# Optimization experiments

Measured on AMD Instinct MI355X. Metric: run time of the kernel, lower is better.

## Reference

```python
import jax, jax.numpy as jnp
from jax import lax
import numpy as np

B, N, C = 8, 16384, 128
NPOINT, NSAMPLE = 1024, 64
RADIUS = 0.3
MLP = [C + 3, 64, 64, 128]  # use_xyz adds 3 input channels


def furthest_point_sample(xyz, npoint):
    """xyz: (B, N, 3) -> inds: (B, npoint) int32, iterative FPS starting at index 0."""
    b, n, _ = xyz.shape
    init_idx = jnp.zeros((b,), jnp.int32)
    mind0 = jnp.full((b, n), 1e10, xyz.dtype)

    def step(carry, _):
        mind, last = carry
        p = jnp.take_along_axis(xyz, last[:, None, None], axis=1)  # (B,1,3)
        d = jnp.sum((xyz - p) ** 2, axis=-1)                       # (B,N)
        mind = jnp.minimum(mind, d)
        nxt = jnp.argmax(mind, axis=-1).astype(jnp.int32)
        return (mind, nxt), nxt

    (_, _), rest = lax.scan(step, (mind0, init_idx), None, length=npoint - 1)
    return jnp.concatenate([init_idx[None], rest], axis=0).T  # (B, npoint)


def ball_query(xyz, new_xyz, radius, nsample):
    """Return (B, npoint, nsample) indices: first nsample points within radius of
    each center; slots past the found count are filled with the first in-ball index
    (matches CUDA ball_query semantics)."""
    n = xyz.shape[1]
    d2 = jnp.sum((new_xyz[:, :, None, :] - xyz[:, None, :, :]) ** 2, axis=-1)  # (B,npoint,N)
    mask = d2 < radius * radius
    score = jnp.where(mask, -jnp.arange(n, dtype=jnp.int32), jnp.int32(-n))
    top, _ = lax.top_k(score, nsample)            # largest scores = smallest valid indices
    idx = -top
    valid = top > -n
    return jnp.where(valid, idx, idx[..., :1])    # pad with first in-ball index


def gather_points(x, idx):
    """x: (B, N, D) or (B, D, N) gathered per batch along point axis via vmap."""
    if x.ndim == 3 and x.shape[-1] != idx.shape[-1]:
        pass
    return x


def reference(xyz, features, W0, b0, W1, b1, W2, b2):
    inds = furthest_point_sample(xyz, NPOINT)                               # (B,npoint)
    new_xyz = jax.vmap(lambda p, i: p[i])(xyz, inds)                        # (B,npoint,3)

    idx = ball_query(xyz, new_xyz, RADIUS, NSAMPLE)                         # (B,npoint,nsample)
    grouped_xyz = jax.vmap(lambda p, i: p[i])(xyz, idx)                     # (B,npoint,nsample,3)
    grouped_xyz = grouped_xyz - new_xyz[:, :, None, :]                      # center-relative
    gx = jnp.transpose(grouped_xyz, (0, 3, 1, 2))                           # (B,3,npoint,nsample)
    gf = jax.vmap(lambda f, i: f[:, i])(features, idx)                      # (B,C,npoint,nsample)
    x = jnp.concatenate([gx, gf], axis=1)                                   # (B,C+3,npoint,nsample)

    # SharedMLP: pointwise Conv2d (1x1) + ReLU per layer
    for W, b in ((W0, b0), (W1, b1), (W2, b2)):
        x = jax.nn.relu(jnp.einsum('bcps,oc->bops', x, W) + b[None, :, None, None])

    new_features = jnp.max(x, axis=-1)                                      # max pool over nsample
    return new_xyz, new_features, inds


def setup_inputs() -> dict:
    key = jax.random.key(0)
    ks = jax.random.split(key, 8)
    inp = {
        'xyz': jax.random.normal(ks[0], (B, N, 3), jnp.float32),
        'features': jax.random.normal(ks[1], (B, C, N), jnp.float32),
    }
    for i in range(3):
        cin, cout = MLP[i], MLP[i + 1]
        inp[f'W{i}'] = jax.random.normal(ks[2 + 2 * i], (cout, cin), jnp.float32) * 0.05
        inp[f'b{i}'] = jax.random.normal(ks[3 + 2 * i], (cout,), jnp.float32) * 0.01
    return inp
```

## Files before the change

kernel.cpp:

```cpp
#include <hip/hip_runtime.h>

#define BATCH   8
#define NPTS    16384
#define NCH     128
#define NPOINT  1024
#define NSAMPLE 64
#define CIN     131

#define THREADS  1024
#define TPP      (NPTS / THREADS)
#define CTAG     0x7C000000u

typedef unsigned long long u64;

__device__ __forceinline__ u64 u64max(u64 a, u64 b) { return a > b ? a : b; }

__device__ __forceinline__ float dpp_wave_max_f32(float v) {
  float o;
  o = __int_as_float(__builtin_amdgcn_update_dpp(
        __float_as_int(v), __float_as_int(v), 0xB1, 0xF, 0xF, false));
  v = fmaxf(v, o);
  o = __int_as_float(__builtin_amdgcn_update_dpp(
        __float_as_int(v), __float_as_int(v), 0x4E, 0xF, 0xF, false));
  v = fmaxf(v, o);
  o = __int_as_float(__builtin_amdgcn_update_dpp(
        __float_as_int(v), __float_as_int(v), 0x141, 0xF, 0xF, false));
  v = fmaxf(v, o);
  o = __int_as_float(__builtin_amdgcn_update_dpp(
        __float_as_int(v), __float_as_int(v), 0x140, 0xF, 0xF, false));
  v = fmaxf(v, o);
  o = __int_as_float(__builtin_amdgcn_update_dpp(
        __float_as_int(v), __float_as_int(v), 0x142, 0xF, 0xF, false));
  v = fmaxf(v, o);
  o = __int_as_float(__builtin_amdgcn_update_dpp(
        __float_as_int(v), __float_as_int(v), 0x143, 0xF, 0xF, false));
  v = fmaxf(v, o);
  return __int_as_float(__builtin_amdgcn_readlane(__float_as_int(v), 63));
}

__device__ __forceinline__ unsigned dpp_wave_min_u32(unsigned v) {
  unsigned o;
  o = (unsigned)__builtin_amdgcn_update_dpp((int)v, (int)v, 0xB1, 0xF, 0xF, false);
  v = min(v, o);
  o = (unsigned)__builtin_amdgcn_update_dpp((int)v, (int)v, 0x4E, 0xF, 0xF, false);
  v = min(v, o);
  o = (unsigned)__builtin_amdgcn_update_dpp((int)v, (int)v, 0x141, 0xF, 0xF, false);
  v = min(v, o);
  o = (unsigned)__builtin_amdgcn_update_dpp((int)v, (int)v, 0x140, 0xF, 0xF, false);
  v = min(v, o);
  o = (unsigned)__builtin_amdgcn_update_dpp((int)v, (int)v, 0x142, 0xF, 0xF, false);
  v = min(v, o);
  o = (unsigned)__builtin_amdgcn_update_dpp((int)v, (int)v, 0x143, 0xF, 0xF, false);
  v = min(v, o);
  return (unsigned)__builtin_amdgcn_readlane((int)v, 63);
}

__global__ void wtrans_kernel(const float* __restrict__ W0,
                              const float* __restrict__ W1,
                              const float* __restrict__ W2,
                              float* __restrict__ w0t,
                              float* __restrict__ w1t,
                              float* __restrict__ w2t)
{
  const int t = blockIdx.x * blockDim.x + threadIdx.x;
  if (t < 64 * CIN) { const int oc = t / CIN, ic = t % CIN; w0t[ic * 64  + oc] = W0[t]; }
  if (t < 64 * 64)  { const int oc = t >> 6,  ic = t & 63;  w1t[ic * 64  + oc] = W1[t]; }
  if (t < 128 * 64) { const int oc = t / 64,  ic = t % 64;  w2t[ic * 128 + oc] = W2[t]; }
}

__global__ __launch_bounds__(THREADS) void mega_kernel(
    const float* __restrict__ xyz, const float* __restrict__ feat,
    const float* __restrict__ w0t, const float* __restrict__ b0,
    const float* __restrict__ w1t, const float* __restrict__ b1,
    const float* __restrict__ w2t, const float* __restrict__ b2,
    float* __restrict__ out_newxyz, float* __restrict__ out_feat,
    float* __restrict__ out_inds_f, u64* __restrict__ cslot)
{
  __shared__ float sA[CIN * 64];
  __shared__ float sB[64 * 64];
  __shared__ int   s_idx[NSAMPLE];
  __shared__ int   bq[4][NSAMPLE];
  __shared__ int   bqcnt[4], bqfirst[4];
  __shared__ u64   s_w[2][16];
  __shared__ unsigned s_sel[4];

  const int t = threadIdx.x;

  if (blockIdx.x < BATCH) {
    const int b = blockIdx.x;
    const int lane = t & 63, wid = t >> 6;
    const float* __restrict__ p = xyz + (size_t)b * NPTS * 3;

    float xs[TPP], ys[TPP], zs[TPP], mind[TPP];
#pragma unroll
    for (int i = 0; i < TPP; ++i) {
      const int n = t + i * THREADS;
      xs[i] = p[n * 3 + 0];
      ys[i] = p[n * 3 + 1];
      zs[i] = p[n * 3 + 2];
      mind[i] = 1e10f;
    }

    u64* __restrict__ cs = cslot + (size_t)b * NPOINT * 4;

    float px = p[0], py = p[1], pz = p[2];
    if (t == 0) {
      out_inds_f[b * NPOINT] = 0.0f;
      const size_t o = (size_t)b * NPOINT * 3;
      out_newxyz[o + 0] = px; out_newxyz[o + 1] = py; out_newxyz[o + 2] = pz;
      const u64 tg = (u64)CTAG << 32;
      __hip_atomic_store(&cs[1], tg | __float_as_uint(px), __ATOMIC_RELAXED, __HIP_MEMORY_SCOPE_AGENT);
      __hip_atomic_store(&cs[2], tg | __float_as_uint(py), __ATOMIC_RELAXED, __HIP_MEMORY_SCOPE_AGENT);
      __hip_atomic_store(&cs[3], tg | __float_as_uint(pz), __ATOMIC_RELAXED, __HIP_MEMORY_SCOPE_AGENT);
      __hip_atomic_store(&cs[0], tg | 0u, __ATOMIC_RELAXED, __HIP_MEMORY_SCOPE_AGENT);
    }

    for (int k = 1; k < NPOINT; ++k) {
      const int par = k & 1;

      float bestv = -1.0f;
      int   besti = 0;
#pragma unroll
      for (int i = 0; i < TPP; ++i) {
        const float dx = xs[i] - px;
        const float dy = ys[i] - py;
        const float dz = zs[i] - pz;
        const float d = __fadd_rn(__fadd_rn(__fmul_rn(dx, dx), __fmul_rn(dy, dy)),
                                  __fmul_rn(dz, dz));
        const float m = fminf(mind[i], d);
        mind[i] = m;
        if (m > bestv) { bestv = m; besti = t + i * THREADS; }
      }

      const float    wmax = dpp_wave_max_f32(bestv);
      const unsigned cand = (bestv == wmax) ? (unsigned)besti : 0xFFFFFFFFu;
      const unsigned widx = dpp_wave_min_u32(cand);

      if (lane == 0)
        s_w[par][wid] = ((u64)__float_as_uint(wmax) << 14)
                      | (u64)((widx ^ 0x3FFFu) & 0x3FFFu);
      __syncthreads();

      u64 a0 = u64max(s_w[par][0],  s_w[par][1]);
      u64 a1 = u64max(s_w[par][2],  s_w[par][3]);
      u64 a2 = u64max(s_w[par][4],  s_w[par][5]);
      u64 a3 = u64max(s_w[par][6],  s_w[par][7]);
      u64 a4 = u64max(s_w[par][8],  s_w[par][9]);
      u64 a5 = u64max(s_w[par][10], s_w[par][11]);
      u64 a6 = u64max(s_w[par][12], s_w[par][13]);
      u64 a7 = u64max(s_w[par][14], s_w[par][15]);
      a0 = u64max(a0, a1); a2 = u64max(a2, a3);
      a4 = u64max(a4, a5); a6 = u64max(a6, a7);
      a0 = u64max(a0, a2); a4 = u64max(a4, a6);
      const u64 bw = u64max(a0, a4);
      const int bi = (int)((bw & 0x3FFF) ^ 0x3FFF);

      px = p[bi * 3 + 0]; py = p[bi * 3 + 1]; pz = p[bi * 3 + 2];

      if (t == 0) {
        out_inds_f[b * NPOINT + k] = (float)bi;
        const size_t o = ((size_t)b * NPOINT + k) * 3;
        out_newxyz[o + 0] = px; out_newxyz[o + 1] = py; out_newxyz[o + 2] = pz;
        const u64 tg = (u64)(CTAG | (unsigned)k) << 32;
        u64* __restrict__ ck = cs + (size_t)k * 4;
        __hip_atomic_store(&ck[1], tg | __float_as_uint(px), __ATOMIC_RELAXED, __HIP_MEMORY_SCOPE_AGENT);
        __hip_atomic_store(&ck[2], tg | __float_as_uint(py), __ATOMIC_RELAXED, __HIP_MEMORY_SCOPE_AGENT);
        __hip_atomic_store(&ck[3], tg | __float_as_uint(pz), __ATOMIC_RELAXED, __HIP_MEMORY_SCOPE_AGENT);
        __hip_atomic_store(&ck[0], tg | (unsigned)bi, __ATOMIC_RELAXED, __HIP_MEMORY_SCOPE_AGENT);
      }
    }
    return;
  }

  const int c  = blockIdx.x - BATCH;
  const int b = c & 7, pc = c >> 3;
  const u64* __restrict__ cs = cslot + ((size_t)b * NPOINT + pc) * 4;

  if (t < 4) {
    const unsigned tg = CTAG | (unsigned)pc;
    u64 v;
    for (;;) {
      v = __hip_atomic_load(cs + t, __ATOMIC_RELAXED, __HIP_MEMORY_SCOPE_AGENT);
      if ((unsigned)(v >> 32) == tg) break;
      __builtin_amdgcn_s_sleep(8);
    }
    s_sel[t] = (unsigned)v;
  }
  __syncthreads();
  const float cx = __uint_as_float(s_sel[1]);
  const float cy = __uint_as_float(s_sel[2]);
  const float cz = __uint_as_float(s_sel[3]);
  const float* __restrict__ pb = xyz + (size_t)b * NPTS * 3;

  if (t < 256) {
    const int w = t >> 6, lane = t & 63;
    const float R2 = (float)(0.3 * 0.3);
    const int beg = w * (NPTS / 4);
    int cnt = 0, first = -1;
    for (int bs = beg; bs < beg + NPTS / 4; bs += 64) {
      const int n = bs + lane;
      const float dx = pb[n * 3 + 0] - cx;
      const float dy = pb[n * 3 + 1] - cy;
      const float dz = pb[n * 3 + 2] - cz;
      const float d = __fadd_rn(__fadd_rn(__fmul_rn(dx, dx), __fmul_rn(dy, dy)),
                                __fmul_rn(dz, dz));
      const bool in = d < R2;
      const u64 m = __ballot(in);
      if (first < 0 && m) first = bs + __ffsll(m) - 1;
      const int pos = __popcll(m & ((1ull << lane) - 1ull));
      if (in && cnt + pos < NSAMPLE) bq[w][cnt + pos] = n;
      cnt += __popcll(m);
      if (cnt >= NSAMPLE) break;
    }
    if (lane == 0) { bqcnt[w] = cnt < NSAMPLE ? cnt : NSAMPLE; bqfirst[w] = first; }
  }
  __syncthreads();
  if (t < NSAMPLE) {
    int firstAll = -1;
#pragma unroll
    for (int w = 0; w < 4; ++w)
      if (firstAll < 0 && bqfirst[w] >= 0) firstAll = bqfirst[w];
    int o = 0, val = -1;
#pragma unroll
    for (int w = 0; w < 4; ++w) {
      const int cw = bqcnt[w];
      if (val < 0 && t >= o && t < o + cw) val = bq[w][t - o];
      o += cw;
    }
    s_idx[t] = (val >= 0) ? val : firstAll;
  }
  __syncthreads();

  const int sm = t & 63, cg = t >> 6;
  const int is = s_idx[sm];
  if (cg == 0) {
    sA[0 * 64 + sm] = pb[is * 3 + 0] - cx;
    sA[1 * 64 + sm] = pb[is * 3 + 1] - cy;
    sA[2 * 64 + sm] = pb[is * 3 + 2] - cz;
  }
  const float* __restrict__ fb = feat + (size_t)b * NCH * NPTS;
  for (int ch = cg; ch < NCH; ch += 16)
    sA[(3 + ch) * 64 + sm] = fb[(size_t)ch * NPTS + is];
  __syncthreads();

  const int s0  = (t & 15) * 4;
  const int oc0 = ((t >> 4) & 15) * 4;

  if (t < 256) {
    float acc[4][4];
#pragma unroll
    for (int j = 0; j < 4; ++j) {
      const float bj = b0[oc0 + j];
#pragma unroll
      for (int i = 0; i < 4; ++i) acc[i][j] = bj;
    }
    for (int ic = 0; ic < CIN; ++ic) {
      const float4 xv = *(const float4*)&sA[ic * 64 + s0];
      const float4 wv = *(const float4*)&w0t[ic * 64 + oc0];
      const float xr[4] = {xv.x, xv.y, xv.z, xv.w};
      const float wr[4] = {wv.x, wv.y, wv.z, wv.w};
#pragma unroll
      for (int i = 0; i < 4; ++i)
#pragma unroll
        for (int j = 0; j < 4; ++j) acc[i][j] += xr[i] * wr[j];
    }
#pragma unroll
    for (int j = 0; j < 4; ++j) {
      float4 r;
      r.x = fmaxf(acc[0][j], 0.f); r.y = fmaxf(acc[1][j], 0.f);
      r.z = fmaxf(acc[2][j], 0.f); r.w = fmaxf(acc[3][j], 0.f);
      *(float4*)&sB[(oc0 + j) * 64 + s0] = r;
    }
  }
  __syncthreads();

  if (t < 256) {
    float acc[4][4];
#pragma unroll
    for (int j = 0; j < 4; ++j) {
      const float bj = b1[oc0 + j];
#pragma unroll
      for (int i = 0; i < 4; ++i) acc[i][j] = bj;
    }
    for (int ic = 0; ic < 64; ++ic) {
      const float4 xv = *(const float4*)&sB[ic * 64 + s0];
      const float4 wv = *(const float4*)&w1t[ic * 64 + oc0];
      const float xr[4] = {xv.x, xv.y, xv.z, xv.w};
      const float wr[4] = {wv.x, wv.y, wv.z, wv.w};
#pragma unroll
      for (int i = 0; i < 4; ++i)
#pragma unroll
        for (int j = 0; j < 4; ++j) acc[i][j] += xr[i] * wr[j];
    }
#pragma unroll
    for (int j = 0; j < 4; ++j) {
      float4 r;
      r.x = fmaxf(acc[0][j], 0.f); r.y = fmaxf(acc[1][j], 0.f);
      r.z = fmaxf(acc[2][j], 0.f); r.w = fmaxf(acc[3][j], 0.f);
      *(float4*)&sA[(oc0 + j) * 64 + s0] = r;
    }
  }
  __syncthreads();

  if (t < 256) {
    const int oc8 = ((t >> 4) & 15) * 8;
    float acc[4][8];
#pragma unroll
    for (int j = 0; j < 8; ++j) {
      const float bj = b2[oc8 + j];
#pragma unroll
      for (int i = 0; i < 4; ++i) acc[i][j] = bj;
    }
    for (int ic = 0; ic < 64; ++ic) {
      const float4 xv  = *(const float4*)&sA[ic * 64 + s0];
      const float4 wlo = *(const float4*)&w2t[ic * 128 + oc8];
      const float4 whi = *(const float4*)&w2t[ic * 128 + oc8 + 4];
      const float xr[4] = {xv.x, xv.y, xv.z, xv.w};
      const float wr[8] = {wlo.x, wlo.y, wlo.z, wlo.w, whi.x, whi.y, whi.z, whi.w};
#pragma unroll
      for (int i = 0; i < 4; ++i)
#pragma unroll
        for (int j = 0; j < 8; ++j) acc[i][j] += xr[i] * wr[j];
    }
    float m[8];
#pragma unroll
    for (int j = 0; j < 8; ++j)
      m[j] = fmaxf(fmaxf(acc[0][j], acc[1][j]), fmaxf(acc[2][j], acc[3][j]));
#pragma unroll
    for (int off = 8; off >= 1; off >>= 1) {
#pragma unroll
      for (int j = 0; j < 8; ++j)
        m[j] = fmaxf(m[j], __shfl_xor(m[j], off, 64));
    }
    if ((t & 15) == 0) {
#pragma unroll
      for (int j = 0; j < 8; ++j)
        out_feat[((size_t)b * NCH + oc8 + j) * NPOINT + pc] = fmaxf(m[j], 0.f);
    }
  }
}

extern "C" void kernel_launch(void* const* d_in, const int* in_sizes, int n_in,
                              void* d_out, int out_size, void* d_ws, size_t ws_size,
                              hipStream_t stream)
{
  const float* xyz  = (const float*)d_in[0];
  const float* feat = (const float*)d_in[1];
  const float* W0   = (const float*)d_in[2];
  const float* b0   = (const float*)d_in[3];
  const float* W1   = (const float*)d_in[4];
  const float* b1   = (const float*)d_in[5];
  const float* W2   = (const float*)d_in[6];
  const float* b2   = (const float*)d_in[7];

  float* out_newxyz = (float*)d_out;
  float* out_feat   = out_newxyz + (size_t)BATCH * NPOINT * 3;
  float* out_inds_f = out_feat + (size_t)BATCH * NCH * NPOINT;

  char* ws = (char*)d_ws;
  u64* cslot = (u64*)ws;
  float* w0t = (float*)(ws + 262144);
  float* w1t = w0t + 64 * CIN;
  float* w2t = w1t + 64 * 64;

  hipMemsetAsync(cslot, 0, 262144, stream);
  wtrans_kernel<<<dim3((64 * CIN + 255) / 256), dim3(256), 0, stream>>>(
      W0, W1, W2, w0t, w1t, w2t);
  mega_kernel<<<dim3(BATCH + BATCH * NPOINT), dim3(THREADS), 0, stream>>>(
      xyz, feat, w0t, b0, w1t, b1, w2t, b2,
      out_newxyz, out_feat, out_inds_f, cslot);
}
```

Measured before the change: 1.985 ms.

## Split furthest point sampling across four cooperating blocks per batch

Each batch's furthest-point-sampling loop now runs on four blocks instead of one, each owning a quarter of the points. Every iteration, each block publishes its local best (distance, index, coordinates) to double-buffered tagged global slots. One wave per block then polls all four slots and picks the global winner, breaking ties toward the lower sub-block. This cuts per-thread distance work and register footprint, but adds an inter-block global-memory handshake and an extra barrier on every one of the roughly thousand serial iterations.

```diff
diff --git a/kernel.cpp b/kernel.cpp
--- a/kernel.cpp
+++ b/kernel.cpp
@@ -7,13 +7,26 @@
 #define NSAMPLE 64
 #define CIN     131
 
-#define THREADS  1024
-#define TPP      (NPTS / THREADS)
-#define CTAG     0x7C000000u
+#define THREADS   1024
+#define FPS_SUBS  4
+#define FPS_CHUNK (NPTS / FPS_SUBS)
+#define TPP       (FPS_CHUNK / THREADS)
+#define CTAG      0x7C000000u
 
 typedef unsigned long long u64;
 
 __device__ __forceinline__ u64 u64max(u64 a, u64 b) { return a > b ? a : b; }
+
+__device__ __forceinline__ u64 shfl_xor_u64(u64 v, int off) {
+  const unsigned lo = __shfl_xor((unsigned)v, off, 64);
+  const unsigned hi = __shfl_xor((unsigned)(v >> 32), off, 64);
+  return ((u64)hi << 32) | lo;
+}
+__device__ __forceinline__ u64 shfl_u64(u64 v, int src) {
+  const unsigned lo = __shfl((unsigned)v, src, 64);
+  const unsigned hi = __shfl((unsigned)(v >> 32), src, 64);
+  return ((u64)hi << 32) | lo;
+}
 
 __device__ __forceinline__ float dpp_wave_max_f32(float v) {
   float o;
@@ -53,6 +66,29 @@
   o = (unsigned)__builtin_amdgcn_update_dpp((int)v, (int)v, 0x143, 0xF, 0xF, false);
   v = min(v, o);
   return (unsigned)__builtin_amdgcn_readlane((int)v, 63);
+}
+
+__device__ __forceinline__ void poll_select(
+    const u64* __restrict__ slots, int k, int lane,
+    float& px, float& py, float& pz, int& widx)
+{
+  const int sub = lane >> 3, word = lane & 7;
+  const bool active = (lane < 32) && (word < 5);
+  u64 v = 0;
+  if (active) {
+    do {
+      v = __hip_atomic_load(slots + sub * 8 + word, __ATOMIC_RELAXED,
+                            __HIP_MEMORY_SCOPE_AGENT);
+    } while ((int)(v >> 32) != k);
+  }
+  u64 key = ((u64)(unsigned)v << 2) | (u64)(3 - (sub & 3));
+  key = u64max(key, shfl_xor_u64(key, 8));
+  key = u64max(key, shfl_xor_u64(key, 16));
+  const int wsub = 3 - (int)(shfl_u64(key, 0) & 3);
+  widx = (int)(unsigned)shfl_u64(v, wsub * 8 + 1);
+  px = __uint_as_float((unsigned)shfl_u64(v, wsub * 8 + 2));
+  py = __uint_as_float((unsigned)shfl_u64(v, wsub * 8 + 3));
+  pz = __uint_as_float((unsigned)shfl_u64(v, wsub * 8 + 4));
 }
 
 __global__ void wtrans_kernel(const float* __restrict__ W0,
@@ -74,37 +110,41 @@
     const float* __restrict__ w1t, const float* __restrict__ b1,
     const float* __restrict__ w2t, const float* __restrict__ b2,
     float* __restrict__ out_newxyz, float* __restrict__ out_feat,
-    float* __restrict__ out_inds_f, u64* __restrict__ cslot)
+    float* __restrict__ out_inds_f,
+    u64* __restrict__ fsync, u64* __restrict__ cslot)
 {
   __shared__ float sA[CIN * 64];
   __shared__ float sB[64 * 64];
   __shared__ int   s_idx[NSAMPLE];
   __shared__ int   bq[4][NSAMPLE];
   __shared__ int   bqcnt[4], bqfirst[4];
-  __shared__ u64   s_w[2][16];
+  __shared__ u64   s_w[16];
   __shared__ unsigned s_sel[4];
 
   const int t = threadIdx.x;
 
-  if (blockIdx.x < BATCH) {
-    const int b = blockIdx.x;
+  if (blockIdx.x < BATCH * FPS_SUBS) {
+    const int bid = blockIdx.x;
+    const int b = bid & 7, sub = bid >> 3;
     const int lane = t & 63, wid = t >> 6;
+    const int base = sub * FPS_CHUNK;
     const float* __restrict__ p = xyz + (size_t)b * NPTS * 3;
 
     float xs[TPP], ys[TPP], zs[TPP], mind[TPP];
 #pragma unroll
     for (int i = 0; i < TPP; ++i) {
-      const int n = t + i * THREADS;
+      const int n = base + t + i * THREADS;
       xs[i] = p[n * 3 + 0];
       ys[i] = p[n * 3 + 1];
       zs[i] = p[n * 3 + 2];
       mind[i] = 1e10f;
     }
 
-    u64* __restrict__ cs = cslot + (size_t)b * NPOINT * 4;
+    u64* __restrict__ slots = fsync + (size_t)b * (2 * FPS_SUBS * 8);
+    u64* __restrict__ cs    = cslot + (size_t)b * NPOINT * 4;
 
     float px = p[0], py = p[1], pz = p[2];
-    if (t == 0) {
+    if (sub == 0 && t == 0) {
       out_inds_f[b * NPOINT] = 0.0f;
       const size_t o = (size_t)b * NPOINT * 3;
       out_newxyz[o + 0] = px; out_newxyz[o + 1] = py; out_newxyz[o + 2] = pz;
@@ -129,50 +169,80 @@
                                   __fmul_rn(dz, dz));
         const float m = fminf(mind[i], d);
         mind[i] = m;
-        if (m > bestv) { bestv = m; besti = t + i * THREADS; }
+        if (m > bestv) { bestv = m; besti = base + t + i * THREADS; }
       }
 
       const float    wmax = dpp_wave_max_f32(bestv);
       const unsigned cand = (bestv == wmax) ? (unsigned)besti : 0xFFFFFFFFu;
-      const unsigned widx = dpp_wave_min_u32(cand);
+      const unsigned wbi  = dpp_wave_min_u32(cand);
 
       if (lane == 0)
-        s_w[par][wid] = ((u64)__float_as_uint(wmax) << 14)
-                      | (u64)((widx ^ 0x3FFFu) & 0x3FFFu);
+        s_w[wid] = ((u64)__float_as_uint(wmax) << 14)
+                 | (u64)((wbi ^ 0x3FFFu) & 0x3FFFu);
       __syncthreads();
 
-      u64 a0 = u64max(s_w[par][0],  s_w[par][1]);
-      u64 a1 = u64max(s_w[par][2],  s_w[par][3]);
-      u64 a2 = u64max(s_w[par][4],  s_w[par][5]);
-      u64 a3 = u64max(s_w[par][6],  s_w[par][7]);
-      u64 a4 = u64max(s_w[par][8],  s_w[par][9]);
-      u64 a5 = u64max(s_w[par][10], s_w[par][11]);
-      u64 a6 = u64max(s_w[par][12], s_w[par][13]);
-      u64 a7 = u64max(s_w[par][14], s_w[par][15]);
+      u64 a0 = u64max(s_w[0],  s_w[1]);
+      u64 a1 = u64max(s_w[2],  s_w[3]);
+      u64 a2 = u64max(s_w[4],  s_w[5]);
+      u64 a3 = u64max(s_w[6],  s_w[7]);
+      u64 a4 = u64max(s_w[8],  s_w[9]);
+      u64 a5 = u64max(s_w[10], s_w[11]);
+      u64 a6 = u64max(s_w[12], s_w[13]);
+      u64 a7 = u64max(s_w[14], s_w[15]);
       a0 = u64max(a0, a1); a2 = u64max(a2, a3);
       a4 = u64max(a4, a5); a6 = u64max(a6, a7);
       a0 = u64max(a0, a2); a4 = u64max(a4, a6);
-      const u64 bw = u64max(a0, a4);
-      const int bi = (int)((bw & 0x3FFF) ^ 0x3FFF);
-
-      px = p[bi * 3 + 0]; py = p[bi * 3 + 1]; pz = p[bi * 3 + 2];
-
-      if (t == 0) {
-        out_inds_f[b * NPOINT + k] = (float)bi;
+      const u64 bw   = u64max(a0, a4);
+      const int bidx = (int)((bw & 0x3FFF) ^ 0x3FFF);
+
+      if (besti == bidx) {
+        const int ii = (bidx - base - t) >> 10;
+        float sx = xs[0], sy = ys[0], sz = zs[0];
+#pragma unroll
+        for (int j = 1; j < TPP; ++j)
+          if (j == ii) { sx = xs[j]; sy = ys[j]; sz = zs[j]; }
+        const u64 tg = (u64)k << 32;
+        u64* __restrict__ sl = slots + par * (FPS_SUBS * 8) + sub * 8;
+        __hip_atomic_store(&sl[0], tg | (unsigned)(bw >> 14), __ATOMIC_RELAXED, __HIP_MEMORY_SCOPE_AGENT);
+        __hip_atomic_store(&sl[1], tg | (unsigned)bidx,       __ATOMIC_RELAXED, __HIP_MEMORY_SCOPE_AGENT);
+        __hip_atomic_store(&sl[2], tg | __float_as_uint(sx),  __ATOMIC_RELAXED, __HIP_MEMORY_SCOPE_AGENT);
+        __hip_atomic_store(&sl[3], tg | __float_as_uint(sy),  __ATOMIC_RELAXED, __HIP_MEMORY_SCOPE_AGENT);
+        __hip_atomic_store(&sl[4], tg | __float_as_uint(sz),  __ATOMIC_RELAXED, __HIP_MEMORY_SCOPE_AGENT);
+      }
+
+      if (wid == 0) {
+        float qx, qy, qz; int widx;
+        poll_select(slots + par * (FPS_SUBS * 8), k, lane, qx, qy, qz, widx);
+        if (lane == 0) {
+          s_sel[0] = (unsigned)widx;
+          s_sel[1] = __float_as_uint(qx);
+          s_sel[2] = __float_as_uint(qy);
+          s_sel[3] = __float_as_uint(qz);
+        }
+      }
+      __syncthreads();
+
+      const int gbi = (int)s_sel[0];
+      px = __uint_as_float(s_sel[1]);
+      py = __uint_as_float(s_sel[2]);
+      pz = __uint_as_float(s_sel[3]);
+
+      if (sub == 0 && t == 0) {
+        out_inds_f[b * NPOINT + k] = (float)gbi;
         const size_t o = ((size_t)b * NPOINT + k) * 3;
         out_newxyz[o + 0] = px; out_newxyz[o + 1] = py; out_newxyz[o + 2] = pz;
         const u64 tg = (u64)(CTAG | (unsigned)k) << 32;
         u64* __restrict__ ck = cs + (size_t)k * 4;
-        __hip_atomic_store(&ck[1], tg | __float_as_uint(px), __ATOMIC_RELAXED, __HIP_MEMORY_SCOPE_AGENT);
-        __hip_atomic_store(&ck[2], tg | __float_as_uint(py), __ATOMIC_RELAXED, __HIP_MEMORY_SCOPE_AGENT);
-        __hip_atomic_store(&ck[3], tg | __float_as_uint(pz), __ATOMIC_RELAXED, __HIP_MEMORY_SCOPE_AGENT);
-        __hip_atomic_store(&ck[0], tg | (unsigned)bi, __ATOMIC_RELAXED, __HIP_MEMORY_SCOPE_AGENT);
+        __hip_atomic_store(&ck[1], tg | s_sel[1], __ATOMIC_RELAXED, __HIP_MEMORY_SCOPE_AGENT);
+        __hip_atomic_store(&ck[2], tg | s_sel[2], __ATOMIC_RELAXED, __HIP_MEMORY_SCOPE_AGENT);
+        __hip_atomic_store(&ck[3], tg | s_sel[3], __ATOMIC_RELAXED, __HIP_MEMORY_SCOPE_AGENT);
+        __hip_atomic_store(&ck[0], tg | (unsigned)gbi, __ATOMIC_RELAXED, __HIP_MEMORY_SCOPE_AGENT);
       }
     }
     return;
   }
 
-  const int c  = blockIdx.x - BATCH;
+  const int c  = blockIdx.x - BATCH * FPS_SUBS;
   const int b = c & 7, pc = c >> 3;
   const u64* __restrict__ cs = cslot + ((size_t)b * NPOINT + pc) * 4;
 
@@ -359,14 +429,15 @@
 
   char* ws = (char*)d_ws;
   u64* cslot = (u64*)ws;
-  float* w0t = (float*)(ws + 262144);
+  u64* fsync = (u64*)(ws + 262144);
+  float* w0t = (float*)(ws + 262144 + 4096);
   float* w1t = w0t + 64 * CIN;
   float* w2t = w1t + 64 * 64;
 
-  hipMemsetAsync(cslot, 0, 262144, stream);
+  hipMemsetAsync(ws, 0, 262144 + 4096, stream);
   wtrans_kernel<<<dim3((64 * CIN + 255) / 256), dim3(256), 0, stream>>>(
       W0, W1, W2, w0t, w1t, w2t);
-  mega_kernel<<<dim3(BATCH + BATCH * NPOINT), dim3(THREADS), 0, stream>>>(
+  mega_kernel<<<dim3(BATCH * FPS_SUBS + BATCH * NPOINT), dim3(THREADS), 0, stream>>>(
       xyz, feat, w0t, b0, w1t, b1, w2t, b2,
-      out_newxyz, out_feat, out_inds_f, cslot);
-}
+      out_newxyz, out_feat, out_inds_f, fsync, cslot);
+}
```

New measurement: 2.436 ms. 1.23x slower.
